# Optimization experiments

Hardware: AMD Instinct MI355X
Metric: run time of the kernel (lower is better)

Reference implementation:

```python
import jax, jax.numpy as jnp
import numpy as np

B, L, F = 256, 512, 64
NUM_IDS = 2000
LN_EPS = 1e-5


def setup_inputs() -> dict:
    key = jax.random.key(0)
    ks = jax.random.split(key, 16)
    s = 0.05
    return {
        # padded neighbor-id sequences; 0 is the padding id
        "src_ids": jax.random.randint(ks[0], (B, L), 0, NUM_IDS, dtype=jnp.int64)
        if jax.config.jax_enable_x64 else jax.random.randint(ks[0], (B, L), 0, NUM_IDS, dtype=jnp.int32),
        "dst_ids": jax.random.randint(ks[1], (B, L), 0, NUM_IDS, dtype=jnp.int64)
        if jax.config.jax_enable_x64 else jax.random.randint(ks[1], (B, L), 0, NUM_IDS, dtype=jnp.int32),
        # co-occurrence encode MLP: Linear(1->F), ReLU, Linear(F->F)
        "enc_w1": jax.random.normal(ks[2], (1, F), jnp.float32) * s,
        "enc_b1": jax.random.normal(ks[3], (F,), jnp.float32) * s,
        "enc_w2": jax.random.normal(ks[4], (F, F), jnp.float32) * s,
        "enc_b2": jax.random.normal(ks[5], (F,), jnp.float32) * s,
        # cross-attention projections (bias-free q/k/v as in source)
        "Wq": jax.random.normal(ks[6], (F, F), jnp.float32) * s,
        "Wk": jax.random.normal(ks[7], (F, F), jnp.float32) * s,
        "Wv": jax.random.normal(ks[8], (F, F), jnp.float32) * s,
        "Wo": jax.random.normal(ks[9], (F, F), jnp.float32) * s,
        "bo": jax.random.normal(ks[10], (F,), jnp.float32) * s,
        "ln_g": jnp.ones((F,), jnp.float32),
        "ln_b": jnp.zeros((F,), jnp.float32),
    }


def _counts_in(a, b):
    # for each element of a: how many times does it occur in b (same batch row)
    # equivalent to the np.unique count / mapping-dict lookup in the original
    return (a[:, :, None] == b[:, None, :]).sum(axis=-1).astype(jnp.float32)


def _appearances(a, b):
    # [B, L, 2]: counts of each id of `a` in (a, b); zero out padding (id==0)
    app = jnp.stack([_counts_in(a, a), _counts_in(a, b)], axis=-1)
    return jnp.where((a == 0)[..., None], 0.0, app)


def _encode(app, w1, b1, w2, b2):
    # Linear(1->F) -> ReLU -> Linear(F->F), then sum over the 2 count channels
    h = jax.nn.relu(app[..., None] * w1[0] + b1)  # [B, L, 2, F]
    h = jnp.einsum('blcf,fg->blcg', h, w2) + b2
    return h.sum(axis=2)  # [B, L, F]


def _linear_attn(q, k, v):
    dim = q.shape[-1]
    q = jax.nn.softmax(q, axis=-1) * (dim ** -0.5)
    k = jax.nn.softmax(k, axis=1)  # softmax over sequence dim (dim=-2)
    ctx = jnp.einsum('bld,ble->bde', k, v)
    return jnp.einsum('bld,bde->ble', q, ctx)


def _layer_norm(x, g, b):
    mu = x.mean(axis=-1, keepdims=True)
    var = ((x - mu) ** 2).mean(axis=-1, keepdims=True)
    return (x - mu) * jax.lax.rsqrt(var + LN_EPS) * g + b


def _cross_attn(x, ctx, Wq, Wk, Wv, Wo, bo, ln_g, ln_b):
    q, k, v = x @ Wq, ctx @ Wk, ctx @ Wv
    attn = _linear_attn(q, k, v)
    return _layer_norm(x + attn @ Wo + bo, ln_g, ln_b)


def reference(src_ids, dst_ids, enc_w1, enc_b1, enc_w2, enc_b2,
              Wq, Wk, Wv, Wo, bo, ln_g, ln_b):
    # neighbor co-occurrence counting + encoding
    src_app = _appearances(src_ids, dst_ids)  # [B, L, 2]
    dst_app = _appearances(dst_ids, src_ids)
    src_feat = _encode(src_app, enc_w1, enc_b1, enc_w2, enc_b2)  # [B, L, F]
    dst_feat = _encode(dst_app, enc_w1, enc_b1, enc_w2, enc_b2)
    # linear cross-attention fusion (shared weights, both directions)
    src_out = _cross_attn(src_feat, dst_feat, Wq, Wk, Wv, Wo, bo, ln_g, ln_b)
    dst_out = _cross_attn(dst_feat, src_feat, Wq, Wk, Wv, Wo, bo, ln_g, ln_b)
    return jnp.stack([src_out, dst_out])  # [2, B, L, F]
```

## Files before the change

kernel.cpp:

```cpp
#include <hip/hip_runtime.h>
#include <hip/hip_bf16.h>

#define BB 256
#define LL 512
#define NIDS 2000

typedef float nfloat4 __attribute__((ext_vector_type(4)));

#define WS_TABLE 0
#define WS_PIDX  32832
#define WS_PKEY  (32832 + 262144)
#define WS_PMULT (32832 + 524288)
#define WS_NPAIR (32832 + 786432)

__global__ __launch_bounds__(256) void k_prep(
    const int* __restrict__ src, const int* __restrict__ dst,
    const float* __restrict__ w1, const float* __restrict__ b1,
    const float* __restrict__ w2, const float* __restrict__ b2,
    float* __restrict__ table,
    int* __restrict__ pidx, int* __restrict__ pkey,
    int* __restrict__ pmult, int* __restrict__ npair) {
  int b = blockIdx.x, tid = threadIdx.x, tx = tid & 63, ty = tid >> 6;
  __shared__ int hs[NIDS], hd[NIDS];
  __shared__ int hkey[1024], hmult[1024], hidx[1024];
  __shared__ float hb[4][64];
  __shared__ int np;

  if (ty < 2 || (b == 255 && ty == 2)) {
    int c = 2 * b + ty;
    hb[ty][tx] = fmaxf((float)c * w1[tx] + b1[tx], 0.f);
    float acc = b2[tx];
#pragma unroll
    for (int f = 0; f < 64; ++f) acc += hb[ty][f] * w2[f * 64 + tx];
    table[c * 64 + tx] = acc;
  }

  for (int i = tid; i < NIDS; i += 256) { hs[i] = 0; hd[i] = 0; }
  __syncthreads();
  const int* s = src + b * LL;
  const int* d = dst + b * LL;
  int sid0 = s[tid], sid1 = s[tid + 256];
  int did0 = d[tid], did1 = d[tid + 256];
  atomicAdd(&hs[sid0], 1); atomicAdd(&hs[sid1], 1);
  atomicAdd(&hd[did0], 1); atomicAdd(&hd[did1], 1);
  __syncthreads();

  for (int side = 0; side < 2; ++side) {
    for (int i = tid; i < 1024; i += 256) { hkey[i] = -1; hmult[i] = 0; }
    if (tid == 0) np = 0;
    __syncthreads();
    int slot[2];
    for (int r = 0; r < 2; ++r) {
      int id = (side == 0) ? (r ? sid1 : sid0) : (r ? did1 : did0);
      int ca = 0, cb = 0;
      if (id != 0) {
        if (side == 0) { ca = hs[id]; cb = hd[id]; }
        else           { ca = hd[id]; cb = hs[id]; }
      }
      int key = ca | (cb << 10);
      int h = (int)(((unsigned)key * 2654435761u) >> 22) & 1023;
      while (true) {
        int old = atomicCAS(&hkey[h], -1, key);
        if (old == -1 || old == key) break;
        h = (h + 1) & 1023;
      }
      atomicAdd(&hmult[h], 1);
      slot[r] = h;
    }
    __syncthreads();
    for (int i = tid; i < 1024; i += 256) {
      if (hkey[i] != -1) {
        int idx = atomicAdd(&np, 1);
        hidx[i] = idx;
        pkey [(side * BB + b) * LL + idx] = hkey[i];
        pmult[(side * BB + b) * LL + idx] = hmult[i];
      }
    }
    __syncthreads();
    pidx[(side * BB + b) * LL + tid]       = hidx[slot[0]];
    pidx[(side * BB + b) * LL + tid + 256] = hidx[slot[1]];
    if (tid == 0) npair[side * BB + b] = np;
    __syncthreads();
  }
}

__global__ __launch_bounds__(256, 3) void k_attn(
    const float* __restrict__ table,
    const int* __restrict__ pidx, const int* __restrict__ pkey,
    const int* __restrict__ pmult, const int* __restrict__ npair,
    const float* __restrict__ Wq, const float* __restrict__ Wk,
    const float* __restrict__ Wv, const float* __restrict__ Wo,
    const float* __restrict__ bo, const float* __restrict__ lng,
    const float* __restrict__ lnb, float* __restrict__ out) {
  int bd = blockIdx.x;
  int b = bd >> 1, dir = bd & 1;
  int tid = threadIdx.x, tx = tid & 63, ty = tid >> 6;

  __shared__ float pool[6144];
  __shared__ float M[64 * 66];
  __shared__ float featb[4][64];
  __shared__ float qbuf[4][64];
  __shared__ float sred[4][64];
  __shared__ int pidxl[512];
  __shared__ int xkeyb[512];
  __shared__ int ckeyb[512];
  __shared__ int cmultb[512];

  int xs = dir, cs = 1 - dir;
  for (int i = tid; i < 512; i += 256) {
    pidxl[i]  = pidx [(xs * BB + b) * LL + i];
    xkeyb[i]  = pkey [(xs * BB + b) * LL + i];
    ckeyb[i]  = pkey [(cs * BB + b) * LL + i];
    cmultb[i] = pmult[(cs * BB + b) * LL + i];
  }
  int Pc = npair[cs * BB + b];
  int Px = npair[xs * BB + b];

  float wa[64];
  float macc[16];
#pragma unroll
  for (int e = 0; e < 16; ++e) macc[e] = 0.f;
  float sacc = 0.f;
  int e0 = ty * 16;
  __syncthreads();

  for (int j0 = 0; j0 < Pc; j0 += 32) {
    int cN = min(32, Pc - j0);
#pragma unroll
    for (int f = 0; f < 64; ++f) wa[f] = Wk[f * 64 + tx];
    for (int j = ty; j < cN; j += 4) {
      int key = ckeyb[j0 + j];
      int ca = key & 1023, cb = key >> 10;
      pool[j * 64 + tx] = table[ca * 64 + tx] + table[cb * 64 + tx];
      float kr = 0.f;
      const float4* fb4 = (const float4*)&pool[j * 64];
#pragma unroll
      for (int q = 0; q < 16; ++q) {
        float4 fv = fb4[q];
        kr += fv.x * wa[4 * q] + fv.y * wa[4 * q + 1] + fv.z * wa[4 * q + 2] + fv.w * wa[4 * q + 3];
      }
      float p = __expf(kr) * (float)cmultb[j0 + j];
      sacc += p;
      pool[2048 + j * 64 + tx] = p;
    }
#pragma unroll
    for (int f = 0; f < 64; ++f) wa[f] = Wv[f * 64 + tx];
    for (int j = ty; j < cN; j += 4) {
      float vr = 0.f;
      const float4* fb4 = (const float4*)&pool[j * 64];
#pragma unroll
      for (int q = 0; q < 16; ++q) {
        float4 fv = fb4[q];
        vr += fv.x * wa[4 * q] + fv.y * wa[4 * q + 1] + fv.z * wa[4 * q + 2] + fv.w * wa[4 * q + 3];
      }
      pool[4096 + j * 64 + tx] = vr;
    }
    __syncthreads();
    for (int jj = 0; jj < cN; ++jj) {
      float pg = pool[2048 + jj * 64 + tx];
      const float4* vb4 = (const float4*)&pool[4096 + jj * 64 + e0];
#pragma unroll
      for (int q = 0; q < 4; ++q) {
        float4 vv = vb4[q];
        macc[4 * q]     += pg * vv.x; macc[4 * q + 1] += pg * vv.y;
        macc[4 * q + 2] += pg * vv.z; macc[4 * q + 3] += pg * vv.w;
      }
    }
    __syncthreads();
  }
  sred[ty][tx] = sacc;
  __syncthreads();
  float inv = 1.f / (sred[0][tx] + sred[1][tx] + sred[2][tx] + sred[3][tx]);
#pragma unroll
  for (int e = 0; e < 16; ++e) M[tx * 66 + e0 + e] = macc[e] * inv;
  for (int i = tid; i < 4096; i += 256) pool[i] = Wo[i];
  __syncthreads();

#pragma unroll
  for (int e = 0; e < 16; ++e) macc[e] = 0.f;
  for (int f = 0; f < 64; ++f) {
    float m = M[tx * 66 + f];
    const float4* wo4 = (const float4*)&pool[f * 64 + e0];
#pragma unroll
    for (int q = 0; q < 4; ++q) {
      float4 w4 = wo4[q];
      macc[4 * q]     += m * w4.x; macc[4 * q + 1] += m * w4.y;
      macc[4 * q + 2] += m * w4.z; macc[4 * q + 3] += m * w4.w;
    }
  }
  __syncthreads();
#pragma unroll
  for (int e = 0; e < 16; ++e) M[tx * 66 + e0 + e] = macc[e];
  __syncthreads();
  float gcol[64];
#pragma unroll
  for (int dd = 0; dd < 64; ++dd) gcol[dd] = M[dd * 66 + tx];
#pragma unroll
  for (int f = 0; f < 64; ++f) wa[f] = Wq[f * 64 + tx];
  float bov = bo[tx], lg = lng[tx], lb = lnb[tx];

  for (int i0 = 0; i0 < Px; i0 += 64) {
    int cN = min(64, Px - i0);
    for (int jj = ty; jj < cN; jj += 4) {
      int key = xkeyb[i0 + jj];
      int ca = key & 1023, cb = key >> 10;
      float fv = table[ca * 64 + tx] + table[cb * 64 + tx];
      featb[ty][tx] = fv;
      float qr = 0.f;
      const float4* fb4 = (const float4*)&featb[ty][0];
#pragma unroll
      for (int q = 0; q < 16; ++q) {
        float4 f4v = fb4[q];
        qr += f4v.x * wa[4 * q] + f4v.y * wa[4 * q + 1] + f4v.z * wa[4 * q + 2] + f4v.w * wa[4 * q + 3];
      }
      float p = __expf(qr);
      float sum = p;
#pragma unroll
      for (int off = 32; off >= 1; off >>= 1) sum += __shfl_xor(sum, off, 64);
      float qh = p / sum * 0.125f;
      qbuf[ty][tx] = qh;
      float at = 0.f;
      const float4* qb4 = (const float4*)&qbuf[ty][0];
#pragma unroll
      for (int q = 0; q < 16; ++q) {
        float4 qv = qb4[q];
        at += qv.x * gcol[4 * q] + qv.y * gcol[4 * q + 1] + qv.z * gcol[4 * q + 2] + qv.w * gcol[4 * q + 3];
      }
      float r = fv + at + bov;
      float mu = r;
#pragma unroll
      for (int off = 32; off >= 1; off >>= 1) mu += __shfl_xor(mu, off, 64);
      mu *= (1.f / 64.f);
      float dv = r - mu;
      float var = dv * dv;
#pragma unroll
      for (int off = 32; off >= 1; off >>= 1) var += __shfl_xor(var, off, 64);
      var *= (1.f / 64.f);
      pool[jj * 64 + tx] = dv * rsqrtf(var + 1e-5f) * lg + lb;
    }
    __syncthreads();
    const nfloat4* w4 = (const nfloat4*)pool;
    nfloat4* out4 = (nfloat4*)(out + (size_t)(dir * BB + b) * (LL * 64));
    for (int idx = tid; idx < 512 * 16; idx += 256) {
      int l = idx >> 4, q = idx & 15;
      int pid = pidxl[l];
      if (pid >= i0 && pid < i0 + cN)
        __builtin_nontemporal_store(w4[(pid - i0) * 16 + q], &out4[l * 16 + q]);
    }
    __syncthreads();
  }
}

extern "C" void kernel_launch(void* const* d_in, const int* in_sizes, int n_in,
                              void* d_out, int out_size, void* d_ws, size_t ws_size,
                              hipStream_t stream) {
  const int* src  = (const int*)d_in[0];
  const int* dst  = (const int*)d_in[1];
  const float* w1 = (const float*)d_in[2];
  const float* b1 = (const float*)d_in[3];
  const float* w2 = (const float*)d_in[4];
  const float* b2 = (const float*)d_in[5];
  const float* Wq = (const float*)d_in[6];
  const float* Wk = (const float*)d_in[7];
  const float* Wv = (const float*)d_in[8];
  const float* Wo = (const float*)d_in[9];
  const float* bo = (const float*)d_in[10];
  const float* lng = (const float*)d_in[11];
  const float* lnb = (const float*)d_in[12];
  float* out = (float*)d_out;
  float* wsf = (float*)d_ws;
  int* wsi = (int*)d_ws;

  float* table = wsf + WS_TABLE;
  int* pidx  = wsi + WS_PIDX;
  int* pkey  = wsi + WS_PKEY;
  int* pmult = wsi + WS_PMULT;
  int* npair = wsi + WS_NPAIR;

  k_prep<<<dim3(256), dim3(256), 0, stream>>>(src, dst, w1, b1, w2, b2,
                                              table, pidx, pkey, pmult, npair);
  k_attn<<<dim3(512), dim3(256), 0, stream>>>(table, pidx, pkey, pmult, npair,
                                              Wq, Wk, Wv, Wo, bo, lng, lnb, out);
}
```

Baseline: 128.9 us.

## Fuse histogram/dedup prep into attention kernel and split table build into tiny kernel

Moves the per-row id histogram and unique-key hashing out of the prep kernel and into the attention kernel, so each (batch, direction) block builds its own keys, multiplicities and pair indices in shared memory instead of writing them to global workspace and reading them back. The encode table gets its own small kernel. Shared memory is overlaid in one buffer, the key/value chunk shrinks from 32 to 16, and the gcol register array is replaced with reads from a transposed shared buffer to relieve register pressure. The cost is that the histogram work is duplicated across the two direction blocks, and the smaller chunk adds more barriers.

```diff
diff --git a/kernel.cpp b/kernel.cpp
--- a/kernel.cpp
+++ b/kernel.cpp
@@ -8,157 +8,164 @@
 typedef float nfloat4 __attribute__((ext_vector_type(4)));
 
 #define WS_TABLE 0
-#define WS_PIDX  32832
-#define WS_PKEY  (32832 + 262144)
-#define WS_PMULT (32832 + 524288)
-#define WS_NPAIR (32832 + 786432)
-
-__global__ __launch_bounds__(256) void k_prep(
-    const int* __restrict__ src, const int* __restrict__ dst,
+
+__global__ __launch_bounds__(64) void k_table(
     const float* __restrict__ w1, const float* __restrict__ b1,
     const float* __restrict__ w2, const float* __restrict__ b2,
-    float* __restrict__ table,
-    int* __restrict__ pidx, int* __restrict__ pkey,
-    int* __restrict__ pmult, int* __restrict__ npair) {
-  int b = blockIdx.x, tid = threadIdx.x, tx = tid & 63, ty = tid >> 6;
-  __shared__ int hs[NIDS], hd[NIDS];
-  __shared__ int hkey[1024], hmult[1024], hidx[1024];
-  __shared__ float hb[4][64];
-  __shared__ int np;
-
-  if (ty < 2 || (b == 255 && ty == 2)) {
-    int c = 2 * b + ty;
-    hb[ty][tx] = fmaxf((float)c * w1[tx] + b1[tx], 0.f);
-    float acc = b2[tx];
-#pragma unroll
-    for (int f = 0; f < 64; ++f) acc += hb[ty][f] * w2[f * 64 + tx];
-    table[c * 64 + tx] = acc;
-  }
-
-  for (int i = tid; i < NIDS; i += 256) { hs[i] = 0; hd[i] = 0; }
-  __syncthreads();
+    float* __restrict__ table) {
+  int c = blockIdx.x, f = threadIdx.x;
+  __shared__ float h[64];
+  h[f] = fmaxf((float)c * w1[f] + b1[f], 0.f);
+  __syncthreads();
+  float acc = b2[f];
+#pragma unroll
+  for (int g = 0; g < 64; ++g) acc += h[g] * w2[g * 64 + f];
+  table[c * 64 + f] = acc;
+}
+
+__global__ __launch_bounds__(256, 3) void k_fused(
+    const int* __restrict__ src, const int* __restrict__ dst,
+    const float* __restrict__ table,
+    const float* __restrict__ Wq, const float* __restrict__ Wk,
+    const float* __restrict__ Wv, const float* __restrict__ Wo,
+    const float* __restrict__ bo, const float* __restrict__ lng,
+    const float* __restrict__ lnb, float* __restrict__ out) {
+  __shared__ __align__(16) char smem[50192];
+  int*   hist  = (int*)smem;
+  float* poolF = (float*)smem;
+  int*   hkey  = (int*)(smem + 16384);
+  int*   hmult = (int*)(smem + 20480);
+  float* fbF   = (float*)(smem + 20480);
+  float* Mg    = (float*)(smem + 24576);
+  int*   xkey  = (int*)(smem + 41984);
+  int*   ckey  = (int*)(smem + 44032);
+  int*   cmult = (int*)(smem + 46080);
+  int*   pidxl = (int*)(smem + 48128);
+  int*   npp   = (int*)(smem + 50176);
+
+  int bd = blockIdx.x, b = bd >> 1, dir = bd & 1;
+  int tid = threadIdx.x, tx = tid & 63, ty = tid >> 6;
+  int e0 = ty * 16;
+
   const int* s = src + b * LL;
   const int* d = dst + b * LL;
   int sid0 = s[tid], sid1 = s[tid + 256];
   int did0 = d[tid], did1 = d[tid + 256];
-  atomicAdd(&hs[sid0], 1); atomicAdd(&hs[sid1], 1);
-  atomicAdd(&hd[did0], 1); atomicAdd(&hd[did1], 1);
-  __syncthreads();
-
-  for (int side = 0; side < 2; ++side) {
-    for (int i = tid; i < 1024; i += 256) { hkey[i] = -1; hmult[i] = 0; }
-    if (tid == 0) np = 0;
-    __syncthreads();
-    int slot[2];
-    for (int r = 0; r < 2; ++r) {
-      int id = (side == 0) ? (r ? sid1 : sid0) : (r ? did1 : did0);
-      int ca = 0, cb = 0;
-      if (id != 0) {
-        if (side == 0) { ca = hs[id]; cb = hd[id]; }
-        else           { ca = hd[id]; cb = hs[id]; }
-      }
-      int key = ca | (cb << 10);
-      int h = (int)(((unsigned)key * 2654435761u) >> 22) & 1023;
-      while (true) {
-        int old = atomicCAS(&hkey[h], -1, key);
-        if (old == -1 || old == key) break;
-        h = (h + 1) & 1023;
-      }
-      atomicAdd(&hmult[h], 1);
-      slot[r] = h;
-    }
-    __syncthreads();
-    for (int i = tid; i < 1024; i += 256) {
-      if (hkey[i] != -1) {
-        int idx = atomicAdd(&np, 1);
-        hidx[i] = idx;
-        pkey [(side * BB + b) * LL + idx] = hkey[i];
-        pmult[(side * BB + b) * LL + idx] = hmult[i];
-      }
-    }
-    __syncthreads();
-    pidx[(side * BB + b) * LL + tid]       = hidx[slot[0]];
-    pidx[(side * BB + b) * LL + tid + 256] = hidx[slot[1]];
-    if (tid == 0) npair[side * BB + b] = np;
-    __syncthreads();
-  }
-}
-
-__global__ __launch_bounds__(256, 3) void k_attn(
-    const float* __restrict__ table,
-    const int* __restrict__ pidx, const int* __restrict__ pkey,
-    const int* __restrict__ pmult, const int* __restrict__ npair,
-    const float* __restrict__ Wq, const float* __restrict__ Wk,
-    const float* __restrict__ Wv, const float* __restrict__ Wo,
-    const float* __restrict__ bo, const float* __restrict__ lng,
-    const float* __restrict__ lnb, float* __restrict__ out) {
-  int bd = blockIdx.x;
-  int b = bd >> 1, dir = bd & 1;
-  int tid = threadIdx.x, tx = tid & 63, ty = tid >> 6;
-
-  __shared__ float pool[6144];
-  __shared__ float M[64 * 66];
-  __shared__ float featb[4][64];
-  __shared__ float qbuf[4][64];
-  __shared__ float sred[4][64];
-  __shared__ int pidxl[512];
-  __shared__ int xkeyb[512];
-  __shared__ int ckeyb[512];
-  __shared__ int cmultb[512];
-
-  int xs = dir, cs = 1 - dir;
-  for (int i = tid; i < 512; i += 256) {
-    pidxl[i]  = pidx [(xs * BB + b) * LL + i];
-    xkeyb[i]  = pkey [(xs * BB + b) * LL + i];
-    ckeyb[i]  = pkey [(cs * BB + b) * LL + i];
-    cmultb[i] = pmult[(cs * BB + b) * LL + i];
-  }
-  int Pc = npair[cs * BB + b];
-  int Px = npair[xs * BB + b];
-
+  for (int i = tid; i < 4000; i += 256) hist[i] = 0;
+  __syncthreads();
+  atomicAdd(&hist[sid0], 1);        atomicAdd(&hist[sid1], 1);
+  atomicAdd(&hist[2000 + did0], 1); atomicAdd(&hist[2000 + did1], 1);
+  __syncthreads();
+
+  int x0 = dir ? did0 : sid0, x1 = dir ? did1 : sid1;
+  int c0 = dir ? sid0 : did0, c1 = dir ? sid1 : did1;
+  const int* hx = dir ? hist + 2000 : hist;
+  const int* hc = dir ? hist : hist + 2000;
+
+  for (int i = tid; i < 1024; i += 256) { hkey[i] = -1; hmult[i] = 0; }
+  if (tid == 0) *npp = 0;
+  __syncthreads();
+  for (int r = 0; r < 2; ++r) {
+    int id = r ? c1 : c0;
+    int ca = 0, cb = 0;
+    if (id != 0) { ca = hc[id]; cb = hx[id]; }
+    int key = ca | (cb << 10);
+    int h = (int)(((unsigned)key * 2654435761u) >> 22) & 1023;
+    while (true) {
+      int old = atomicCAS(&hkey[h], -1, key);
+      if (old == -1 || old == key) break;
+      h = (h + 1) & 1023;
+    }
+    atomicAdd(&hmult[h], 1);
+  }
+  __syncthreads();
+  for (int i = tid; i < 1024; i += 256) {
+    if (hkey[i] != -1) {
+      int idx = atomicAdd(npp, 1);
+      ckey[idx]  = hkey[i];
+      cmult[idx] = hmult[i];
+    }
+  }
+  __syncthreads();
+  int Pc = *npp;
+  __syncthreads();
+
+  for (int i = tid; i < 1024; i += 256) { hkey[i] = -1; hmult[i] = 0; }
+  if (tid == 0) *npp = 0;
+  __syncthreads();
+  int slot0, slot1;
+  for (int r = 0; r < 2; ++r) {
+    int id = r ? x1 : x0;
+    int ca = 0, cb = 0;
+    if (id != 0) { ca = hx[id]; cb = hc[id]; }
+    int key = ca | (cb << 10);
+    int h = (int)(((unsigned)key * 2654435761u) >> 22) & 1023;
+    while (true) {
+      int old = atomicCAS(&hkey[h], -1, key);
+      if (old == -1 || old == key) break;
+      h = (h + 1) & 1023;
+    }
+    if (r) slot1 = h; else slot0 = h;
+  }
+  __syncthreads();
+  for (int i = tid; i < 1024; i += 256) {
+    int k = hkey[i];
+    if (k != -1) {
+      int idx = atomicAdd(npp, 1);
+      xkey[idx] = k;
+      hkey[i] = idx;
+    }
+  }
+  __syncthreads();
+  pidxl[tid]       = hkey[slot0];
+  pidxl[tid + 256] = hkey[slot1];
+  int Px = *npp;
+  __syncthreads();
+
+  float* featA = poolF;
+  float* pA    = poolF + 1024;
+  float* vA    = poolF + 2048;
   float wa[64];
   float macc[16];
 #pragma unroll
   for (int e = 0; e < 16; ++e) macc[e] = 0.f;
   float sacc = 0.f;
-  int e0 = ty * 16;
-  __syncthreads();
-
-  for (int j0 = 0; j0 < Pc; j0 += 32) {
-    int cN = min(32, Pc - j0);
+
+  for (int j0 = 0; j0 < Pc; j0 += 16) {
+    int cN = min(16, Pc - j0);
 #pragma unroll
     for (int f = 0; f < 64; ++f) wa[f] = Wk[f * 64 + tx];
     for (int j = ty; j < cN; j += 4) {
-      int key = ckeyb[j0 + j];
+      int key = ckey[j0 + j];
       int ca = key & 1023, cb = key >> 10;
-      pool[j * 64 + tx] = table[ca * 64 + tx] + table[cb * 64 + tx];
+      featA[j * 64 + tx] = table[ca * 64 + tx] + table[cb * 64 + tx];
       float kr = 0.f;
-      const float4* fb4 = (const float4*)&pool[j * 64];
+      const float4* fb4 = (const float4*)&featA[j * 64];
 #pragma unroll
       for (int q = 0; q < 16; ++q) {
         float4 fv = fb4[q];
         kr += fv.x * wa[4 * q] + fv.y * wa[4 * q + 1] + fv.z * wa[4 * q + 2] + fv.w * wa[4 * q + 3];
       }
-      float p = __expf(kr) * (float)cmultb[j0 + j];
+      float p = __expf(kr) * (float)cmult[j0 + j];
       sacc += p;
-      pool[2048 + j * 64 + tx] = p;
+      pA[j * 64 + tx] = p;
     }
 #pragma unroll
     for (int f = 0; f < 64; ++f) wa[f] = Wv[f * 64 + tx];
     for (int j = ty; j < cN; j += 4) {
       float vr = 0.f;
-      const float4* fb4 = (const float4*)&pool[j * 64];
+      const float4* fb4 = (const float4*)&featA[j * 64];
 #pragma unroll
       for (int q = 0; q < 16; ++q) {
         float4 fv = fb4[q];
         vr += fv.x * wa[4 * q] + fv.y * wa[4 * q + 1] + fv.z * wa[4 * q + 2] + fv.w * wa[4 * q + 3];
       }
-      pool[4096 + j * 64 + tx] = vr;
+      vA[j * 64 + tx] = vr;
     }
     __syncthreads();
     for (int jj = 0; jj < cN; ++jj) {
-      float pg = pool[2048 + jj * 64 + tx];
-      const float4* vb4 = (const float4*)&pool[4096 + jj * 64 + e0];
+      float pg = pA[jj * 64 + tx];
+      const float4* vb4 = (const float4*)&vA[jj * 64 + e0];
 #pragma unroll
       for (int q = 0; q < 4; ++q) {
         float4 vv = vb4[q];
@@ -168,46 +175,43 @@
     }
     __syncthreads();
   }
-  sred[ty][tx] = sacc;
-  __syncthreads();
-  float inv = 1.f / (sred[0][tx] + sred[1][tx] + sred[2][tx] + sred[3][tx]);
-#pragma unroll
-  for (int e = 0; e < 16; ++e) M[tx * 66 + e0 + e] = macc[e] * inv;
-  for (int i = tid; i < 4096; i += 256) pool[i] = Wo[i];
+  fbF[512 + ty * 64 + tx] = sacc;
+  __syncthreads();
+  float inv = 1.f / (fbF[512 + tx] + fbF[576 + tx] + fbF[640 + tx] + fbF[704 + tx]);
+#pragma unroll
+  for (int e = 0; e < 16; ++e) Mg[(e0 + e) * 68 + tx] = macc[e] * inv;
+  for (int i = tid; i < 4096; i += 256) poolF[i] = Wo[i];
+#pragma unroll
+  for (int f = 0; f < 64; ++f) wa[f] = Wq[f * 64 + tx];
+  float bov = bo[tx], lg = lng[tx], lb = lnb[tx];
   __syncthreads();
 
 #pragma unroll
   for (int e = 0; e < 16; ++e) macc[e] = 0.f;
   for (int f = 0; f < 64; ++f) {
-    float m = M[tx * 66 + f];
-    const float4* wo4 = (const float4*)&pool[f * 64 + e0];
+    float mt = Mg[f * 68 + tx];
+    const float4* wo4 = (const float4*)&poolF[f * 64 + e0];
 #pragma unroll
     for (int q = 0; q < 4; ++q) {
       float4 w4 = wo4[q];
-      macc[4 * q]     += m * w4.x; macc[4 * q + 1] += m * w4.y;
-      macc[4 * q + 2] += m * w4.z; macc[4 * q + 3] += m * w4.w;
-    }
-  }
-  __syncthreads();
-#pragma unroll
-  for (int e = 0; e < 16; ++e) M[tx * 66 + e0 + e] = macc[e];
-  __syncthreads();
-  float gcol[64];
-#pragma unroll
-  for (int dd = 0; dd < 64; ++dd) gcol[dd] = M[dd * 66 + tx];
-#pragma unroll
-  for (int f = 0; f < 64; ++f) wa[f] = Wq[f * 64 + tx];
-  float bov = bo[tx], lg = lng[tx], lb = lnb[tx];
+      macc[4 * q]     += mt * w4.x; macc[4 * q + 1] += mt * w4.y;
+      macc[4 * q + 2] += mt * w4.z; macc[4 * q + 3] += mt * w4.w;
+    }
+  }
+  __syncthreads();
+#pragma unroll
+  for (int e = 0; e < 16; ++e) Mg[(e0 + e) * 68 + tx] = macc[e];
+  __syncthreads();
 
   for (int i0 = 0; i0 < Px; i0 += 64) {
     int cN = min(64, Px - i0);
     for (int jj = ty; jj < cN; jj += 4) {
-      int key = xkeyb[i0 + jj];
+      int key = xkey[i0 + jj];
       int ca = key & 1023, cb = key >> 10;
       float fv = table[ca * 64 + tx] + table[cb * 64 + tx];
-      featb[ty][tx] = fv;
+      fbF[ty * 64 + tx] = fv;
       float qr = 0.f;
-      const float4* fb4 = (const float4*)&featb[ty][0];
+      const float4* fb4 = (const float4*)&fbF[ty * 64];
 #pragma unroll
       for (int q = 0; q < 16; ++q) {
         float4 f4v = fb4[q];
@@ -218,13 +222,15 @@
 #pragma unroll
       for (int off = 32; off >= 1; off >>= 1) sum += __shfl_xor(sum, off, 64);
       float qh = p / sum * 0.125f;
-      qbuf[ty][tx] = qh;
+      fbF[256 + ty * 64 + tx] = qh;
       float at = 0.f;
-      const float4* qb4 = (const float4*)&qbuf[ty][0];
+      const float4* qb4 = (const float4*)&fbF[256 + ty * 64];
+      const float4* gt4 = (const float4*)&Mg[tx * 68];
 #pragma unroll
       for (int q = 0; q < 16; ++q) {
         float4 qv = qb4[q];
-        at += qv.x * gcol[4 * q] + qv.y * gcol[4 * q + 1] + qv.z * gcol[4 * q + 2] + qv.w * gcol[4 * q + 3];
+        float4 gv = gt4[q];
+        at += qv.x * gv.x + qv.y * gv.y + qv.z * gv.z + qv.w * gv.w;
       }
       float r = fv + at + bov;
       float mu = r;
@@ -236,10 +242,10 @@
 #pragma unroll
       for (int off = 32; off >= 1; off >>= 1) var += __shfl_xor(var, off, 64);
       var *= (1.f / 64.f);
-      pool[jj * 64 + tx] = dv * rsqrtf(var + 1e-5f) * lg + lb;
-    }
-    __syncthreads();
-    const nfloat4* w4 = (const nfloat4*)pool;
+      poolF[jj * 64 + tx] = dv * rsqrtf(var + 1e-5f) * lg + lb;
+    }
+    __syncthreads();
+    const nfloat4* w4 = (const nfloat4*)poolF;
     nfloat4* out4 = (nfloat4*)(out + (size_t)(dir * BB + b) * (LL * 64));
     for (int idx = tid; idx < 512 * 16; idx += 256) {
       int l = idx >> 4, q = idx & 15;
@@ -268,17 +274,9 @@
   const float* lng = (const float*)d_in[11];
   const float* lnb = (const float*)d_in[12];
   float* out = (float*)d_out;
-  float* wsf = (float*)d_ws;
-  int* wsi = (int*)d_ws;
-
-  float* table = wsf + WS_TABLE;
-  int* pidx  = wsi + WS_PIDX;
-  int* pkey  = wsi + WS_PKEY;
-  int* pmult = wsi + WS_PMULT;
-  int* npair = wsi + WS_NPAIR;
-
-  k_prep<<<dim3(256), dim3(256), 0, stream>>>(src, dst, w1, b1, w2, b2,
-                                              table, pidx, pkey, pmult, npair);
-  k_attn<<<dim3(512), dim3(256), 0, stream>>>(table, pidx, pkey, pmult, npair,
-                                              Wq, Wk, Wv, Wo, bo, lng, lnb, out);
+  float* table = (float*)d_ws + WS_TABLE;
+
+  k_table<<<dim3(513), dim3(64), 0, stream>>>(w1, b1, w2, b2, table);
+  k_fused<<<dim3(512), dim3(256), 0, stream>>>(src, dst, table,
+                                               Wq, Wk, Wv, Wo, bo, lng, lnb, out);
 }
```

After: 129.8 us. No clear change (+0.7%).
